# Kernel optimization log

Measured on AMD Instinct MI355X. Metric: run time of the kernel, lower is better.

Reference implementation:

```python
import jax, jax.numpy as jnp
import numpy as np

N_HEADS = 4
NUM_GROUPS = 32
EPS = 1e-6


def _nin(t, W, b):
    # 1x1 conv as dense over channel dim: [B,C,H,W] x [C,D] -> [B,D,H,W]
    return jnp.einsum('bchw,cd->bdhw', t, W) + b[None, :, None, None]


def setup_inputs() -> dict:
    key = jax.random.key(0)
    ks = jax.random.split(key, 12)
    B, C, H, W = 8, 256, 32, 32
    Tc = 512
    Cin = C + Tc  # 768
    x = jax.random.normal(ks[0], (B, C, H, W), dtype=jnp.float32)
    text_feat = jax.random.normal(ks[1], (B, Tc), dtype=jnp.float32)
    gn_gamma = jnp.ones((Cin,), dtype=jnp.float32)
    gn_beta = jnp.zeros((Cin,), dtype=jnp.float32)
    scale = 1.0 / np.sqrt(Cin)
    W0 = jax.random.normal(ks[2], (Cin, C), dtype=jnp.float32) * scale
    b0 = jnp.zeros((C,), dtype=jnp.float32)
    W1 = jax.random.normal(ks[3], (Cin, C), dtype=jnp.float32) * scale
    b1 = jnp.zeros((C,), dtype=jnp.float32)
    W2 = jax.random.normal(ks[4], (Cin, C), dtype=jnp.float32) * scale
    b2 = jnp.zeros((C,), dtype=jnp.float32)
    return {"x": x, "text_feat": text_feat, "gn_gamma": gn_gamma, "gn_beta": gn_beta,
            "W0": W0, "b0": b0, "W1": W1, "b1": b1, "W2": W2, "b2": b2}


def reference(x, text_feat, gn_gamma, gn_beta, W0, b0, W1, b1, W2, b2):
    B, C, H, W = x.shape
    # broadcast text features spatially and concat on channel dim
    tf = jnp.broadcast_to(text_feat[:, :, None, None], (B, text_feat.shape[1], H, W))
    h = jnp.concatenate([x, tf], axis=1)  # [B, C+Tc, H, W]
    Ctot = h.shape[1]
    # GroupNorm(32, Ctot), eps=1e-6
    hg = h.reshape(B, NUM_GROUPS, Ctot // NUM_GROUPS, H, W)
    mu = hg.mean(axis=(2, 3, 4), keepdims=True)
    var = hg.var(axis=(2, 3, 4), keepdims=True)
    hn = ((hg - mu) * jax.lax.rsqrt(var + EPS)).reshape(B, Ctot, H, W)
    hn = hn * gn_gamma[None, :, None, None] + gn_beta[None, :, None, None]
    q = _nin(hn, W0, b0)
    k = _nin(hn, W1, b1)
    v = _nin(hn, W2, b2)
    Ch = C // N_HEADS
    qh = q.reshape(B * N_HEADS, Ch, H, W)
    kh = k.reshape(B * N_HEADS, Ch, H, W)
    vh = v.reshape(B * N_HEADS, Ch, H, W)
    # full HW x HW attention scores, softmax over flattened key positions
    w = jnp.einsum('bchw,bcij->bhwij', qh, kh) * (Ch ** -0.5)
    w = jax.nn.softmax(w.reshape(B * N_HEADS, H, W, H * W), axis=-1)
    w = w.reshape(B * N_HEADS, H, W, H, W)
    ho = jnp.einsum('bhwij,bcij->bchw', w, vh).reshape(B, C, H, W)
    return x + ho
```

## Files before the change

### kernel.cpp

```cpp
#include <hip/hip_runtime.h>
#include <math.h>

#define BATCH 8
#define CX 256
#define TC 512
#define CIN 768
#define HW_TOT 1024
#define NH 4
#define CHD 64
#define SPLIT 4

typedef __attribute__((ext_vector_type(8))) short short8;
typedef __attribute__((ext_vector_type(4))) short s4v;
typedef __attribute__((ext_vector_type(4))) float floatx4;

static __device__ __forceinline__ short f2bf(float f) {
    union { float f; unsigned u; } c; c.f = f;
    unsigned r = (c.u + 0x7fffu + ((c.u >> 16) & 1u)) >> 16;
    return (short)r;
}

__global__ __launch_bounds__(256)
void gn_kernel(const float* __restrict__ x, const float* __restrict__ tf,
               const float* __restrict__ gamma, const float* __restrict__ beta,
               float* __restrict__ scale, float* __restrict__ shift,
               float* __restrict__ tc) {
    const int b = blockIdx.x >> 5;
    const int g = blockIdx.x & 31;
    const int t = threadIdx.x;
    const int w = t >> 6, lane = t & 63;
    if (blockIdx.x < 24) tc[blockIdx.x * 256 + t] = 0.f;

    float s = 0.f, ss = 0.f;
    #pragma unroll
    for (int rr = 0; rr < 6; rr++) {
        const int row = w * 6 + rr;
        const int cg = g * 24 + row;
        if (cg < CX) {
            const float4* p = (const float4*)(x + ((size_t)b * CX + cg) * HW_TOT);
            #pragma unroll
            for (int i = 0; i < 4; i++) {
                float4 v = p[lane + 64 * i];
                s += v.x + v.y + v.z + v.w;
                ss += v.x * v.x + v.y * v.y + v.z * v.z + v.w * v.w;
            }
        } else {
            float v = tf[b * TC + cg - CX];
            s += 16.f * v;
            ss += 16.f * v * v;
        }
    }
    #pragma unroll
    for (int d = 1; d < 64; d <<= 1) {
        s += __shfl_xor(s, d);
        ss += __shfl_xor(ss, d);
    }
    __shared__ float rs_[4], rss_[4];
    if (lane == 0) { rs_[w] = s; rss_[w] = ss; }
    __syncthreads();
    const float S  = rs_[0] + rs_[1] + rs_[2] + rs_[3];
    const float SS = rss_[0] + rss_[1] + rss_[2] + rss_[3];
    const float inv_n = 1.f / (24 * 1024);
    const float mean = S * inv_n;
    const float var = SS * inv_n - mean * mean;
    const float r = rsqrtf(var + 1e-6f);
    if (t < 24) {
        int cg = g * 24 + t;
        float sc = gamma[cg] * r;
        scale[b * CIN + cg] = sc;
        shift[b * CIN + cg] = beta[cg] - mean * sc;
    }
}

__global__ __launch_bounds__(256)
void prep_kernel(const float* __restrict__ x, const float* __restrict__ tf,
                 const float* __restrict__ scale, const float* __restrict__ shift,
                 const float* __restrict__ W0, const float* __restrict__ W1,
                 const float* __restrict__ W2,
                 short* __restrict__ hnT, short* __restrict__ Wt,
                 float* __restrict__ tc) {
    __shared__ float hs[128];
    __shared__ float red[4][64];
    const int bx = blockIdx.x;
    const int t = threadIdx.x;
    if (bx < 256) {
        int id = (bx & 31) * 256 + t;
        int b = id >> 10;
        const float* xb = x + (size_t)b * CX * HW_TOT + (id & 1023);
        const float* scb = scale + b * CIN;
        const float* shb = shift + b * CIN;
        short* outp = hnT + (size_t)id * CX;
        int c0base = (bx >> 5) * 32;
        for (int c0 = c0base; c0 < c0base + 32; c0 += 8) {
            short8 o;
            #pragma unroll
            for (int i = 0; i < 8; i++) {
                float v = xb[(size_t)(c0 + i) * HW_TOT];
                o[i] = f2bf(v * scb[c0 + i] + shb[c0 + i]);
            }
            *(short8*)(outp + c0) = o;
        }
    } else if (bx < 268) {
        int m = bx - 256;
        int dg = (m % 3) * 256 + t;
        int which = dg >> 8, d = dg & 255;
        const float* Wm = (which == 0) ? W0 : (which == 1) ? W1 : W2;
        int c0base = (m / 3) * 64;
        for (int c0 = c0base; c0 < c0base + 64; c0 += 8) {
            short8 o;
            #pragma unroll
            for (int i = 0; i < 8; i++) o[i] = f2bf(Wm[(size_t)(c0 + i) * CX + d]);
            *(short8*)(Wt + (size_t)dg * CX + c0) = o;
        }
    } else {
        int m = bx - 268;
        int ks = m & 3;
        int b = (m >> 2) & 7, dt = m >> 5;
        int which = dt >> 2, d0 = (dt & 3) * 64;
        const float* Wm = (which == 0) ? W0 : (which == 1) ? W1 : W2;
        if (t < 128) {
            int c = ks * 128 + t;
            hs[t] = tf[b * TC + c] * scale[b * CIN + CX + c] + shift[b * CIN + CX + c];
        }
        __syncthreads();
        int td = t & 63, tq = t >> 6;
        float acc = 0.f;
        const float* wp = Wm + (size_t)(CX + ks * 128 + tq * 32) * CX + d0 + td;
        #pragma unroll 8
        for (int c = 0; c < 32; c++)
            acc = fmaf(hs[tq * 32 + c], wp[(size_t)c * CX], acc);
        red[tq][td] = acc;
        __syncthreads();
        if (t < 64)
            atomicAdd(&tc[b * CIN + which * CX + d0 + t],
                      red[0][t] + red[1][t] + red[2][t] + red[3][t]);
    }
}

__global__ __launch_bounds__(256)
void qkv_gemm(const short* __restrict__ hnT, const short* __restrict__ Wt,
              const float* __restrict__ tc,
              const float* __restrict__ b0, const float* __restrict__ b1,
              const float* __restrict__ b2,
              short* __restrict__ qb, short* __restrict__ kb, short* __restrict__ vb) {
    const int hw0 = blockIdx.x * 64, dt = blockIdx.y, b = blockIdx.z;
    const int which = dt >> 2;
    const int col0 = (dt & 3) * 64;
    const int dg0 = which * 256 + col0;
    const bool OV = (which == 2);

    __shared__ short At[64 * 72];
    __shared__ short Bt[64 * 72];

    const int t = threadIdx.x;
    const int w = t >> 6, l = t & 63;
    const int wm = w >> 1, wn = w & 1;
    const int l15 = l & 15, q = l >> 4;
    const int srow = t >> 2, sch = (t & 3) * 16;

    const short* gA = hnT + (size_t)(b * HW_TOT + hw0 + srow) * CX + sch;
    const short* gB = Wt + (size_t)(dg0 + srow) * CX + sch;

    floatx4 acc[2][2] = {};
    for (int k0 = 0; k0 < CX; k0 += 64) {
        __syncthreads();
        *(short8*)(At + srow * 72 + sch)     = *(const short8*)(gA + k0);
        *(short8*)(At + srow * 72 + sch + 8) = *(const short8*)(gA + k0 + 8);
        *(short8*)(Bt + srow * 72 + sch)     = *(const short8*)(gB + k0);
        *(short8*)(Bt + srow * 72 + sch + 8) = *(const short8*)(gB + k0 + 8);
        __syncthreads();
        const short* aB = OV ? Bt : At;
        const short* bB = OV ? At : Bt;
        #pragma unroll
        for (int kc = 0; kc < 2; kc++) {
            short8 af[2], bf2[2];
            #pragma unroll
            for (int mt = 0; mt < 2; mt++)
                af[mt] = *(const short8*)(aB + (wm * 32 + mt * 16 + l15) * 72 + kc * 32 + q * 8);
            #pragma unroll
            for (int nt = 0; nt < 2; nt++)
                bf2[nt] = *(const short8*)(bB + (wn * 32 + nt * 16 + l15) * 72 + kc * 32 + q * 8);
            #pragma unroll
            for (int mt = 0; mt < 2; mt++)
                #pragma unroll
                for (int nt = 0; nt < 2; nt++)
                    acc[mt][nt] = __builtin_amdgcn_mfma_f32_16x16x32_bf16(
                        af[mt], bf2[nt], acc[mt][nt], 0, 0, 0);
        }
    }

    __syncthreads();
    const float* bias = (which == 0) ? b0 : (which == 1) ? b1 : b2;
    if (!OV) {
        float cadd[2];
        #pragma unroll
        for (int nt = 0; nt < 2; nt++) {
            int d = col0 + wn * 32 + nt * 16 + l15;
            cadd[nt] = bias[d] + tc[b * CIN + which * CX + d];
        }
        #pragma unroll
        for (int mt = 0; mt < 2; mt++)
            #pragma unroll
            for (int rr = 0; rr < 4; rr++)
                #pragma unroll
                for (int nt = 0; nt < 2; nt++)
                    At[(wm * 32 + mt * 16 + q * 4 + rr) * 72 + wn * 32 + nt * 16 + l15]
                        = f2bf(acc[mt][nt][rr] + cadd[nt]);
    } else {
        #pragma unroll
        for (int mt = 0; mt < 2; mt++)
            #pragma unroll
            for (int rr = 0; rr < 4; rr++) {
                int d = col0 + wm * 32 + mt * 16 + q * 4 + rr;
                float radd = bias[d] + tc[b * CIN + 2 * CX + d];
                #pragma unroll
                for (int nt = 0; nt < 2; nt++)
                    At[(wm * 32 + mt * 16 + q * 4 + rr) * 72 + wn * 32 + nt * 16 + l15]
                        = f2bf(acc[mt][nt][rr] + radd);
            }
    }
    __syncthreads();
    short8 v0 = *(const short8*)(At + srow * 72 + sch);
    short8 v1 = *(const short8*)(At + srow * 72 + sch + 8);
    if (!OV) {
        short* outp = (which == 0) ? qb : kb;
        size_t off = (size_t)(b * HW_TOT + hw0 + srow) * CX + col0 + sch;
        *(short8*)(outp + off) = v0;
        *(short8*)(outp + off + 8) = v1;
    } else {
        size_t off = (size_t)(b * CX + col0 + srow) * HW_TOT + hw0 + sch;
        *(short8*)(vb + off) = v0;
        *(short8*)(vb + off + 8) = v1;
    }
}

__global__ __launch_bounds__(256)
void attn_part(const short* __restrict__ qb, const short* __restrict__ kb,
               const short* __restrict__ vb,
               float* __restrict__ opart, float* __restrict__ lpart) {
    const int qt = blockIdx.x, bh = blockIdx.y, sp = blockIdx.z;
    const int b = bh >> 2, h = bh & 3;
    const int hw0 = qt * 64;

    __shared__ short Qs[64 * 72];
    __shared__ short Ks[64 * 72];
    __shared__ short Vs[64 * 72];

    const int t = threadIdx.x;
    const int w = t >> 6, l = t & 63;
    const int l15 = l & 15, q = l >> 4;
    const int srow = t >> 2, sch = (t & 3) * 16;

    {
        const short* gq = qb + (size_t)(b * HW_TOT + hw0 + srow) * CX + h * CHD + sch;
        *(short8*)(Qs + srow * 72 + sch)     = *(const short8*)gq;
        *(short8*)(Qs + srow * 72 + sch + 8) = *(const short8*)(gq + 8);
    }

    short8 pk0, pk1, pv0, pv1;
    {
        const int j0 = sp * (HW_TOT / SPLIT);
        const short* gk = kb + (size_t)(b * HW_TOT + j0 + srow) * CX + h * CHD + sch;
        pk0 = *(const short8*)gk;
        pk1 = *(const short8*)(gk + 8);
        const short* gv = vb + (size_t)(b * CX + h * CHD + srow) * HW_TOT + j0 + sch;
        pv0 = *(const short8*)gv;
        pv1 = *(const short8*)(gv + 8);
    }
    __syncthreads();
    const short8 aq0 = *(const short8*)(Qs + (w * 16 + l15) * 72 + q * 8);
    const short8 aq1 = *(const short8*)(Qs + (w * 16 + l15) * 72 + 32 + q * 8);

    floatx4 oacc[4] = {};
    float lsum = 0.f;

    for (int jj = 0; jj < HW_TOT / SPLIT / 64; jj++) {
        *(short8*)(Ks + srow * 72 + sch)     = pk0;
        *(short8*)(Ks + srow * 72 + sch + 8) = pk1;
        *(short8*)(Vs + srow * 72 + sch)     = pv0;
        *(short8*)(Vs + srow * 72 + sch + 8) = pv1;
        __syncthreads();

        if (jj < HW_TOT / SPLIT / 64 - 1) {
            const int j0 = sp * (HW_TOT / SPLIT) + (jj + 1) * 64;
            const short* gk = kb + (size_t)(b * HW_TOT + j0 + srow) * CX + h * CHD + sch;
            pk0 = *(const short8*)gk;
            pk1 = *(const short8*)(gk + 8);
            const short* gv = vb + (size_t)(b * CX + h * CHD + srow) * HW_TOT + j0 + sch;
            pv0 = *(const short8*)gv;
            pv1 = *(const short8*)(gv + 8);
        }

        floatx4 sacc[4] = {};
        #pragma unroll
        for (int nt = 0; nt < 4; nt++) {
            short8 kf0 = *(const short8*)(Ks + (nt * 16 + l15) * 72 + q * 8);
            short8 kf1 = *(const short8*)(Ks + (nt * 16 + l15) * 72 + 32 + q * 8);
            sacc[nt] = __builtin_amdgcn_mfma_f32_16x16x32_bf16(kf0, aq0, sacc[nt], 0, 0, 0);
            sacc[nt] = __builtin_amdgcn_mfma_f32_16x16x32_bf16(kf1, aq1, sacc[nt], 0, 0, 0);
        }

        short8 pf[2];
        #pragma unroll
        for (int nt = 0; nt < 4; nt++)
            #pragma unroll
            for (int r = 0; r < 4; r++) {
                float e = __expf(fmaf(sacc[nt][r], 0.125f, -10.f));
                lsum += e;
                pf[nt >> 1][(nt & 1) * 4 + r] = f2bf(e);
            }

        #pragma unroll
        for (int ct = 0; ct < 4; ct++) {
            const short* vr = Vs + (ct * 16 + l15) * 72;
            #pragma unroll
            for (int kcc = 0; kcc < 2; kcc++) {
                s4v vlo = *(const s4v*)(vr + kcc * 32 + q * 4);
                s4v vhi = *(const s4v*)(vr + kcc * 32 + 16 + q * 4);
                short8 vf = __builtin_shufflevector(vlo, vhi, 0, 1, 2, 3, 4, 5, 6, 7);
                oacc[ct] = __builtin_amdgcn_mfma_f32_16x16x32_bf16(vf, pf[kcc], oacc[ct], 0, 0, 0);
            }
        }
        __syncthreads();
    }

    float* op = opart + ((size_t)(sp * BATCH + b) * CX) * HW_TOT;
    #pragma unroll
    for (int ct = 0; ct < 4; ct++)
        #pragma unroll
        for (int r = 0; r < 4; r++) {
            int c = h * CHD + ct * 16 + q * 4 + r;
            op[(size_t)c * HW_TOT + hw0 + w * 16 + l15] = oacc[ct][r];
        }
    lsum += __shfl_xor(lsum, 16);
    lsum += __shfl_xor(lsum, 32);
    if (q == 0)
        lpart[(size_t)(sp * 32 + bh) * HW_TOT + hw0 + w * 16 + l15] = lsum;
}

__global__ __launch_bounds__(256)
void attn_epi(const float* __restrict__ opart, const float* __restrict__ lpart,
              const float* __restrict__ x, float* __restrict__ out) {
    const int idx = (blockIdx.x * 256 + threadIdx.x) * 4;
    const int b = idx >> 18, c = (idx >> 10) & 255, hw = idx & 1023;
    const int bh = b * 4 + (c >> 6);
    const size_t lo = (size_t)bh * HW_TOT + hw;
    float4 osum = make_float4(0.f, 0.f, 0.f, 0.f);
    float4 lsum = make_float4(0.f, 0.f, 0.f, 0.f);
    #pragma unroll
    for (int s = 0; s < SPLIT; s++) {
        float4 o = *(const float4*)(opart + (size_t)s * BATCH * CX * HW_TOT + idx);
        float4 lv = *(const float4*)(lpart + (size_t)s * 32 * HW_TOT + lo);
        osum.x += o.x; osum.y += o.y; osum.z += o.z; osum.w += o.w;
        lsum.x += lv.x; lsum.y += lv.y; lsum.z += lv.z; lsum.w += lv.w;
    }
    float4 xv = *(const float4*)(x + idx);
    float4 ov;
    ov.x = xv.x + osum.x / lsum.x;
    ov.y = xv.y + osum.y / lsum.y;
    ov.z = xv.z + osum.z / lsum.z;
    ov.w = xv.w + osum.w / lsum.w;
    *(float4*)(out + idx) = ov;
}

extern "C" void kernel_launch(void* const* d_in, const int* in_sizes, int n_in,
                              void* d_out, int out_size, void* d_ws, size_t ws_size,
                              hipStream_t stream) {
    (void)in_sizes; (void)n_in; (void)out_size; (void)ws_size;
    const float* x     = (const float*)d_in[0];
    const float* tf    = (const float*)d_in[1];
    const float* gamma = (const float*)d_in[2];
    const float* beta  = (const float*)d_in[3];
    const float* W0 = (const float*)d_in[4];
    const float* b0 = (const float*)d_in[5];
    const float* W1 = (const float*)d_in[6];
    const float* b1 = (const float*)d_in[7];
    const float* W2 = (const float*)d_in[8];
    const float* b2 = (const float*)d_in[9];

    char* ws = (char*)d_ws;
    float* scale  = (float*)(ws);
    float* shift  = (float*)(ws + 24576);
    float* tcb    = (float*)(ws + 49152);
    short* Wt     = (short*)(ws + 73728);
    short* hnT    = (short*)(ws + 466944);
    short* qb     = (short*)(ws + 4661248);
    short* kb     = (short*)(ws + 8855552);
    short* vb     = (short*)(ws + 13049856);
    float* opart  = (float*)(ws + 17244160);
    float* lpart  = (float*)(ws + 50798592);

    hipLaunchKernelGGL(gn_kernel, dim3(256), dim3(256), 0, stream,
                       x, tf, gamma, beta, scale, shift, tcb);
    hipLaunchKernelGGL(prep_kernel, dim3(652), dim3(256), 0, stream,
                       x, tf, scale, shift, W0, W1, W2, hnT, Wt, tcb);
    hipLaunchKernelGGL(qkv_gemm, dim3(16, 12, BATCH), dim3(256), 0, stream,
                       hnT, Wt, tcb, b0, b1, b2, qb, kb, vb);
    hipLaunchKernelGGL(attn_part, dim3(16, 32, SPLIT), dim3(256), 0, stream,
                       qb, kb, vb, opart, lpart);
    hipLaunchKernelGGL(attn_epi, dim3(2048), dim3(256), 0, stream,
                       opart, lpart, x, (float*)d_out);
}
```

Before: 129.4 us.

## Fuse attention split-K and epilogue into one double-buffered kernel

Removes the 4-way key split and the separate reduction/epilogue kernel. Each block now walks all 1024 keys and writes out = x + o/l directly. This avoids writing and re-reading roughly 33MB of fp32 partials and saves a launch. The K/V LDS tiles are double-buffered, so there is one barrier per iteration instead of two. The exp is switched to exp2 with prescaled constants, and bf16 packing uses truncation instead of round-to-nearest. In exchange the grid shrinks from 2048 to 512 blocks, which may underfill the 256 CUs. The truncated P values add a small precision change.

```diff
diff --git a/kernel.cpp b/kernel.cpp
--- a/kernel.cpp
+++ b/kernel.cpp
@@ -8,16 +8,22 @@
 #define HW_TOT 1024
 #define NH 4
 #define CHD 64
-#define SPLIT 4
 
 typedef __attribute__((ext_vector_type(8))) short short8;
 typedef __attribute__((ext_vector_type(4))) short s4v;
 typedef __attribute__((ext_vector_type(4))) float floatx4;
+typedef __attribute__((ext_vector_type(4))) int int4v;
 
 static __device__ __forceinline__ short f2bf(float f) {
     union { float f; unsigned u; } c; c.f = f;
     unsigned r = (c.u + 0x7fffu + ((c.u >> 16) & 1u)) >> 16;
     return (short)r;
+}
+
+static __device__ __forceinline__ int pack_trunc(float lo, float hi) {
+    union { float f; unsigned u; } L, H;
+    L.f = lo; H.f = hi;
+    return (int)((H.u & 0xffff0000u) | (L.u >> 16));
 }
 
 __global__ __launch_bounds__(256)
@@ -235,16 +241,16 @@
 }
 
 __global__ __launch_bounds__(256)
-void attn_part(const short* __restrict__ qb, const short* __restrict__ kb,
-               const short* __restrict__ vb,
-               float* __restrict__ opart, float* __restrict__ lpart) {
-    const int qt = blockIdx.x, bh = blockIdx.y, sp = blockIdx.z;
+void attn_kernel(const short* __restrict__ qb, const short* __restrict__ kb,
+                 const short* __restrict__ vb, const float* __restrict__ x,
+                 float* __restrict__ out) {
+    const int qt = blockIdx.x, bh = blockIdx.y;
     const int b = bh >> 2, h = bh & 3;
     const int hw0 = qt * 64;
 
     __shared__ short Qs[64 * 72];
-    __shared__ short Ks[64 * 72];
-    __shared__ short Vs[64 * 72];
+    __shared__ short Ks[2][64 * 72];
+    __shared__ short Vs[2][64 * 72];
 
     const int t = threadIdx.x;
     const int w = t >> 6, l = t & 63;
@@ -259,13 +265,16 @@
 
     short8 pk0, pk1, pv0, pv1;
     {
-        const int j0 = sp * (HW_TOT / SPLIT);
-        const short* gk = kb + (size_t)(b * HW_TOT + j0 + srow) * CX + h * CHD + sch;
+        const short* gk = kb + (size_t)(b * HW_TOT + 0 + srow) * CX + h * CHD + sch;
         pk0 = *(const short8*)gk;
         pk1 = *(const short8*)(gk + 8);
-        const short* gv = vb + (size_t)(b * CX + h * CHD + srow) * HW_TOT + j0 + sch;
+        const short* gv = vb + (size_t)(b * CX + h * CHD + srow) * HW_TOT + 0 + sch;
         pv0 = *(const short8*)gv;
         pv1 = *(const short8*)(gv + 8);
+        *(short8*)(Ks[0] + srow * 72 + sch)     = pk0;
+        *(short8*)(Ks[0] + srow * 72 + sch + 8) = pk1;
+        *(short8*)(Vs[0] + srow * 72 + sch)     = pv0;
+        *(short8*)(Vs[0] + srow * 72 + sch + 8) = pv1;
     }
     __syncthreads();
     const short8 aq0 = *(const short8*)(Qs + (w * 16 + l15) * 72 + q * 8);
@@ -273,16 +282,13 @@
 
     floatx4 oacc[4] = {};
     float lsum = 0.f;
-
-    for (int jj = 0; jj < HW_TOT / SPLIT / 64; jj++) {
-        *(short8*)(Ks + srow * 72 + sch)     = pk0;
-        *(short8*)(Ks + srow * 72 + sch + 8) = pk1;
-        *(short8*)(Vs + srow * 72 + sch)     = pv0;
-        *(short8*)(Vs + srow * 72 + sch + 8) = pv1;
-        __syncthreads();
-
-        if (jj < HW_TOT / SPLIT / 64 - 1) {
-            const int j0 = sp * (HW_TOT / SPLIT) + (jj + 1) * 64;
+    const float C1 = 0.125f * 1.44269504f;
+    const float C2 = -10.f * 1.44269504f;
+
+    for (int jj = 0; jj < 16; jj++) {
+        const int cur = jj & 1;
+        if (jj < 15) {
+            const int j0 = (jj + 1) * 64;
             const short* gk = kb + (size_t)(b * HW_TOT + j0 + srow) * CX + h * CHD + sch;
             pk0 = *(const short8*)gk;
             pk1 = *(const short8*)(gk + 8);
@@ -291,76 +297,69 @@
             pv1 = *(const short8*)(gv + 8);
         }
 
+        const short* Kc = Ks[cur];
         floatx4 sacc[4] = {};
         #pragma unroll
         for (int nt = 0; nt < 4; nt++) {
-            short8 kf0 = *(const short8*)(Ks + (nt * 16 + l15) * 72 + q * 8);
-            short8 kf1 = *(const short8*)(Ks + (nt * 16 + l15) * 72 + 32 + q * 8);
+            short8 kf0 = *(const short8*)(Kc + (nt * 16 + l15) * 72 + q * 8);
+            short8 kf1 = *(const short8*)(Kc + (nt * 16 + l15) * 72 + 32 + q * 8);
             sacc[nt] = __builtin_amdgcn_mfma_f32_16x16x32_bf16(kf0, aq0, sacc[nt], 0, 0, 0);
             sacc[nt] = __builtin_amdgcn_mfma_f32_16x16x32_bf16(kf1, aq1, sacc[nt], 0, 0, 0);
         }
 
-        short8 pf[2];
+        float ev[4][4];
         #pragma unroll
         for (int nt = 0; nt < 4; nt++)
             #pragma unroll
             for (int r = 0; r < 4; r++) {
-                float e = __expf(fmaf(sacc[nt][r], 0.125f, -10.f));
+                float e = exp2f(fmaf(sacc[nt][r], C1, C2));
+                ev[nt][r] = e;
                 lsum += e;
-                pf[nt >> 1][(nt & 1) * 4 + r] = f2bf(e);
-            }
-
+            }
+        union { int4v i; short8 s; } u0, u1;
+        u0.i[0] = pack_trunc(ev[0][0], ev[0][1]);
+        u0.i[1] = pack_trunc(ev[0][2], ev[0][3]);
+        u0.i[2] = pack_trunc(ev[1][0], ev[1][1]);
+        u0.i[3] = pack_trunc(ev[1][2], ev[1][3]);
+        u1.i[0] = pack_trunc(ev[2][0], ev[2][1]);
+        u1.i[1] = pack_trunc(ev[2][2], ev[2][3]);
+        u1.i[2] = pack_trunc(ev[3][0], ev[3][1]);
+        u1.i[3] = pack_trunc(ev[3][2], ev[3][3]);
+
+        const short* Vc = Vs[cur];
         #pragma unroll
         for (int ct = 0; ct < 4; ct++) {
-            const short* vr = Vs + (ct * 16 + l15) * 72;
+            const short* vr = Vc + (ct * 16 + l15) * 72;
             #pragma unroll
             for (int kcc = 0; kcc < 2; kcc++) {
                 s4v vlo = *(const s4v*)(vr + kcc * 32 + q * 4);
                 s4v vhi = *(const s4v*)(vr + kcc * 32 + 16 + q * 4);
                 short8 vf = __builtin_shufflevector(vlo, vhi, 0, 1, 2, 3, 4, 5, 6, 7);
-                oacc[ct] = __builtin_amdgcn_mfma_f32_16x16x32_bf16(vf, pf[kcc], oacc[ct], 0, 0, 0);
-            }
-        }
-        __syncthreads();
-    }
-
-    float* op = opart + ((size_t)(sp * BATCH + b) * CX) * HW_TOT;
+                oacc[ct] = __builtin_amdgcn_mfma_f32_16x16x32_bf16(
+                    vf, kcc ? u1.s : u0.s, oacc[ct], 0, 0, 0);
+            }
+        }
+
+        if (jj < 15) {
+            *(short8*)(Ks[1 - cur] + srow * 72 + sch)     = pk0;
+            *(short8*)(Ks[1 - cur] + srow * 72 + sch + 8) = pk1;
+            *(short8*)(Vs[1 - cur] + srow * 72 + sch)     = pv0;
+            *(short8*)(Vs[1 - cur] + srow * 72 + sch + 8) = pv1;
+            __syncthreads();
+        }
+    }
+
+    lsum += __shfl_xor(lsum, 16);
+    lsum += __shfl_xor(lsum, 32);
+    const float rinv = 1.f / lsum;
     #pragma unroll
     for (int ct = 0; ct < 4; ct++)
         #pragma unroll
         for (int r = 0; r < 4; r++) {
             int c = h * CHD + ct * 16 + q * 4 + r;
-            op[(size_t)c * HW_TOT + hw0 + w * 16 + l15] = oacc[ct][r];
-        }
-    lsum += __shfl_xor(lsum, 16);
-    lsum += __shfl_xor(lsum, 32);
-    if (q == 0)
-        lpart[(size_t)(sp * 32 + bh) * HW_TOT + hw0 + w * 16 + l15] = lsum;
-}
-
-__global__ __launch_bounds__(256)
-void attn_epi(const float* __restrict__ opart, const float* __restrict__ lpart,
-              const float* __restrict__ x, float* __restrict__ out) {
-    const int idx = (blockIdx.x * 256 + threadIdx.x) * 4;
-    const int b = idx >> 18, c = (idx >> 10) & 255, hw = idx & 1023;
-    const int bh = b * 4 + (c >> 6);
-    const size_t lo = (size_t)bh * HW_TOT + hw;
-    float4 osum = make_float4(0.f, 0.f, 0.f, 0.f);
-    float4 lsum = make_float4(0.f, 0.f, 0.f, 0.f);
-    #pragma unroll
-    for (int s = 0; s < SPLIT; s++) {
-        float4 o = *(const float4*)(opart + (size_t)s * BATCH * CX * HW_TOT + idx);
-        float4 lv = *(const float4*)(lpart + (size_t)s * 32 * HW_TOT + lo);
-        osum.x += o.x; osum.y += o.y; osum.z += o.z; osum.w += o.w;
-        lsum.x += lv.x; lsum.y += lv.y; lsum.z += lv.z; lsum.w += lv.w;
-    }
-    float4 xv = *(const float4*)(x + idx);
-    float4 ov;
-    ov.x = xv.x + osum.x / lsum.x;
-    ov.y = xv.y + osum.y / lsum.y;
-    ov.z = xv.z + osum.z / lsum.z;
-    ov.w = xv.w + osum.w / lsum.w;
-    *(float4*)(out + idx) = ov;
+            size_t idx = (size_t)(b * CX + c) * HW_TOT + hw0 + w * 16 + l15;
+            out[idx] = x[idx] + oacc[ct][r] * rinv;
+        }
 }
 
 extern "C" void kernel_launch(void* const* d_in, const int* in_sizes, int n_in,
@@ -387,8 +386,6 @@
     short* qb     = (short*)(ws + 4661248);
     short* kb     = (short*)(ws + 8855552);
     short* vb     = (short*)(ws + 13049856);
-    float* opart  = (float*)(ws + 17244160);
-    float* lpart  = (float*)(ws + 50798592);
 
     hipLaunchKernelGGL(gn_kernel, dim3(256), dim3(256), 0, stream,
                        x, tf, gamma, beta, scale, shift, tcb);
@@ -396,8 +393,6 @@
                        x, tf, scale, shift, W0, W1, W2, hnT, Wt, tcb);
     hipLaunchKernelGGL(qkv_gemm, dim3(16, 12, BATCH), dim3(256), 0, stream,
                        hnT, Wt, tcb, b0, b1, b2, qb, kb, vb);
-    hipLaunchKernelGGL(attn_part, dim3(16, 32, SPLIT), dim3(256), 0, stream,
-                       qb, kb, vb, opart, lpart);
-    hipLaunchKernelGGL(attn_epi, dim3(2048), dim3(256), 0, stream,
-                       opart, lpart, x, (float*)d_out);
-}
+    hipLaunchKernelGGL(attn_kernel, dim3(16, 32), dim3(256), 0, stream,
+                       qb, kb, vb, x, (float*)d_out);
+}
```

New measurement: 121.1 us. -6.4%, faster.
